# Kernel tuning notes

Hardware: AMD Instinct MI355X
Metric: run time of the kernel (lower is better)

Reference implementation:

```python
import jax, jax.numpy as jnp
import numpy as np

# opt constants baked from init_kwargs
OPT_M = 1024      # number of OFDM subcarriers (opt.M)
N_PILOT = 0       # opt.N_pilot
VELOCITY = 100.0  # opt.V (is_random_v=False)
DECAY = 4.0       # opt.decay
C_LIGHT = 3.0e8
CARRIER_FREQ = 3.0e9


def setup_inputs() -> dict:
    key = jax.random.key(0)
    k1, k2 = jax.random.split(key, 2)
    N, P, L, M, S = 16, 4, 16, OPT_M, 128
    # channel tap power profile: exp(-l/decay), normalized
    power = jnp.exp(-jnp.arange(L, dtype=jnp.float32) / DECAY)
    power = power / jnp.sum(power)
    # Rayleigh(sigma=1) samples = sqrt(g1^2 + g2^2), g_i ~ N(0,1)
    g = jax.random.normal(k1, (N, P, L, 2), dtype=jnp.float32)
    rayleigh = jnp.sqrt(g[..., 0] ** 2 + g[..., 1] ** 2)
    cof = jnp.sqrt(power / 2.0) * rayleigh  # (N,P,L), strictly positive
    input_ri = jax.random.normal(k2, (N, P, S * M, 2), dtype=jnp.float32)
    return {"input_ri": input_ri, "cof": cof, "Ns": 128}


def reference(input_ri, cof, Ns):
    N, P, SMK, _ = input_ri.shape
    L = cof.shape[-1]
    S = Ns + N_PILOT  # OFDM mode: S = Ns + N_pilot, M = opt.M
    Mk = SMK // S
    x = (input_ri[..., 0] + 1j * input_ri[..., 1]).astype(jnp.complex64)  # (N,P,SMK)

    # per-tap propagation delay from tap gain: len = -100*log(cof); delay1 = len/c
    delay1 = (-100.0 * jnp.log(cof)) / C_LIGHT                      # (N,P,L)
    delay2 = jnp.linspace(0.0, (S - 1) * (0.0005 / 14.0), S).astype(jnp.float32)  # (S,)
    delay = delay1[..., None] + delay2                              # (N,P,L,S)

    max_doppler = VELOCITY / C_LIGHT * CARRIER_FREQ
    angles = jnp.linspace(0.0, 2.0 * np.pi, L).astype(jnp.float32)  # (L,)
    phase_coef = (2.0 * np.pi * jnp.cos(angles) * max_doppler)      # (L,)
    phases = phase_coef[None, None, :, None] * delay                # (N,P,L,S)
    shift = jnp.exp(-1j * phases.astype(jnp.float32))               # complex64 (N,P,L,S)

    # sum over taps L BEFORE multiplying by the L-independent input (same math,
    # avoids materializing the (N,P,L,S,M) broadcast intermediate)
    factor = jnp.sum(cof[..., None].astype(jnp.complex64) * shift, axis=2)  # (N,P,S)
    out = x.reshape(N, P, S, Mk) * factor[..., None]                # (N,P,S,M)
    out = out.reshape(N, P, SMK)
    out_ri = jnp.stack([out.real, out.imag], axis=-1)               # (N,P,SMK,2)

    # frequency response H_t = FFT of zero-padded taps
    cof_zp = jnp.concatenate([cof, jnp.zeros((N, P, OPT_M - L), cof.dtype)], axis=-1)
    H_t = jnp.fft.fft(cof_zp.astype(jnp.complex64), axis=-1)        # (N,P,OPT_M)
    H_t_ri = jnp.stack([H_t.real, H_t.imag], axis=-1)
    return out_ri, H_t_ri
```

## Files before the change

### kernel.cpp

```cpp
#include <hip/hip_runtime.h>
#include <math.h>

#define NB     16
#define PB     4
#define LTAPS  16
#define SS     128
#define MM     1024

#define TWO_PI_F 6.28318530717958647692f

#define HT_BLKS     256
#define STREAM_BLKS 2048
#define TOT4 (NB * PB * SS * MM / 2)

typedef float f32x4 __attribute__((ext_vector_type(4)));
typedef float f32x2 __attribute__((ext_vector_type(2)));

__global__ __launch_bounds__(256) void fused_kernel(
    const float* __restrict__ in,
    const float* __restrict__ cof,
    float* __restrict__ out,
    float* __restrict__ ht)
{
    const int b = blockIdx.x;
    const int t = threadIdx.x;

    if (b >= HT_BLKS) {
        const int sb = b - HT_BLKS;
        __shared__ float term_re[64], term_im[64];
        __shared__ f32x2 facs[4];

        if (t < 64) {
            const int j  = t >> 4;
            const int l  = t & 15;
            const int id = sb * 4 + j;
            const int np = id >> 7;
            const int s  = id & (SS - 1);
            const float cofl   = cof[np * LTAPS + l];
            const float delay1 = (-100.0f / 3.0e8f) * logf(cofl);
            const float delay2 = (0.0005f / 14.0f) * (float)s;
            const float pc     = TWO_PI_F * 1000.0f * cosf((TWO_PI_F / 15.0f) * (float)l);
            const float ph     = pc * (delay1 + delay2);
            float sn, cs;
            sincosf(ph, &sn, &cs);
            term_re[t] = cofl * cs;
            term_im[t] = -cofl * sn;
        }
        __syncthreads();
        if (t < 4) {
            float re = 0.0f, im = 0.0f;
#pragma unroll
            for (int l = 0; l < LTAPS; ++l) {
                re += term_re[t * 16 + l];
                im += term_im[t * 16 + l];
            }
            f32x2 f; f.x = re; f.y = im;
            facs[t] = f;
        }
        __syncthreads();

        const f32x4* __restrict__ in4  = (const f32x4*)in + (size_t)sb * 2048;
        f32x4* __restrict__       out4 = (f32x4*)out      + (size_t)sb * 2048;
#pragma unroll
        for (int k = 0; k < 8; ++k) {
            const int   idx = k * 256 + t;
            const f32x2 f   = facs[k >> 1];
            const f32x4 v   = __builtin_nontemporal_load(&in4[idx]);
            f32x4 r;
            r.x = v.x * f.x - v.y * f.y;
            r.y = v.x * f.y + v.y * f.x;
            r.z = v.z * f.x - v.w * f.y;
            r.w = v.z * f.y + v.w * f.x;
            __builtin_nontemporal_store(r, &out4[idx]);
        }
    } else {
        const int id = b * 256 + t;
        const int np = id >> 10;
        const int k  = id & (MM - 1);
        float sn, cs;
        sincosf((TWO_PI_F / (float)MM) * (float)k, &sn, &cs);
        const float wr = cs, wi = -sn;
        const float* __restrict__ c = cof + np * LTAPS;
        float hr = 0.0f, hi = 0.0f;
        float cr = 1.0f, ci = 0.0f;
#pragma unroll
        for (int l = 0; l < LTAPS; ++l) {
            const float cl = c[l];
            hr += cl * cr;
            hi += cl * ci;
            const float nr = cr * wr - ci * wi;
            const float ni = cr * wi + ci * wr;
            cr = nr; ci = ni;
        }
        float2* __restrict__ o = (float2*)ht;
        o[id] = make_float2(hr, hi);
    }
}

extern "C" void kernel_launch(void* const* d_in, const int* in_sizes, int n_in,
                              void* d_out, int out_size, void* d_ws, size_t ws_size,
                              hipStream_t stream)
{
    const float* in  = (const float*)d_in[0];
    const float* cof = (const float*)d_in[1];
    float* out = (float*)d_out;
    float* ht  = out + (size_t)NB * PB * SS * MM * 2;

    hipLaunchKernelGGL(fused_kernel, dim3(HT_BLKS + STREAM_BLKS), dim3(256), 0, stream,
                       in, cof, out, ht);
}
```

Before: 26.59 us.

## Issue input loads before factor computation and replace LDS reduction with wave shuffles

Each streaming block now issues all eight nontemporal 16-byte loads up front, then has every wavefront redundantly compute the four per-symbol tap sums with xor-shuffle reductions instead of shared memory and two barriers. This overlaps the transcendental factor computation with memory latency and removes block-wide synchronisation. The cost is redundant log/sincos work in all four waves and more live registers to hold the loaded vectors.

```diff
diff --git a/kernel.cpp b/kernel.cpp
--- a/kernel.cpp
+++ b/kernel.cpp
@@ -14,7 +14,6 @@
 #define TOT4 (NB * PB * SS * MM / 2)
 
 typedef float f32x4 __attribute__((ext_vector_type(4)));
-typedef float f32x2 __attribute__((ext_vector_type(2)));
 
 __global__ __launch_bounds__(256) void fused_kernel(
     const float* __restrict__ in,
@@ -27,51 +26,50 @@
 
     if (b >= HT_BLKS) {
         const int sb = b - HT_BLKS;
-        __shared__ float term_re[64], term_im[64];
-        __shared__ f32x2 facs[4];
-
-        if (t < 64) {
-            const int j  = t >> 4;
-            const int l  = t & 15;
-            const int id = sb * 4 + j;
-            const int np = id >> 7;
-            const int s  = id & (SS - 1);
-            const float cofl   = cof[np * LTAPS + l];
-            const float delay1 = (-100.0f / 3.0e8f) * logf(cofl);
-            const float delay2 = (0.0005f / 14.0f) * (float)s;
-            const float pc     = TWO_PI_F * 1000.0f * cosf((TWO_PI_F / 15.0f) * (float)l);
-            const float ph     = pc * (delay1 + delay2);
-            float sn, cs;
-            sincosf(ph, &sn, &cs);
-            term_re[t] = cofl * cs;
-            term_im[t] = -cofl * sn;
-        }
-        __syncthreads();
-        if (t < 4) {
-            float re = 0.0f, im = 0.0f;
-#pragma unroll
-            for (int l = 0; l < LTAPS; ++l) {
-                re += term_re[t * 16 + l];
-                im += term_im[t * 16 + l];
-            }
-            f32x2 f; f.x = re; f.y = im;
-            facs[t] = f;
-        }
-        __syncthreads();
 
         const f32x4* __restrict__ in4  = (const f32x4*)in + (size_t)sb * 2048;
         f32x4* __restrict__       out4 = (f32x4*)out      + (size_t)sb * 2048;
+        f32x4 v[8];
+#pragma unroll
+        for (int k = 0; k < 8; ++k)
+            v[k] = __builtin_nontemporal_load(&in4[k * 256 + t]);
+
+        const int lane = t & 63;
+        const int j    = lane >> 4;
+        const int l    = lane & 15;
+        const int id   = sb * 4 + j;
+        const int np   = id >> 7;
+        const int s    = id & (SS - 1);
+        const float cofl   = cof[np * LTAPS + l];
+        const float delay1 = (-100.0f / 3.0e8f) * logf(cofl);
+        const float delay2 = (0.0005f / 14.0f) * (float)s;
+        const float pc     = TWO_PI_F * 1000.0f * cosf((TWO_PI_F / 15.0f) * (float)l);
+        const float ph     = pc * (delay1 + delay2);
+        float sn, cs;
+        sincosf(ph, &sn, &cs);
+        float re = cofl * cs;
+        float im = -cofl * sn;
+#pragma unroll
+        for (int w = 1; w < 16; w <<= 1) {
+            re += __shfl_xor(re, w);
+            im += __shfl_xor(im, w);
+        }
+        float fre[4], fim[4];
+#pragma unroll
+        for (int jj = 0; jj < 4; ++jj) {
+            fre[jj] = __shfl(re, jj * 16);
+            fim[jj] = __shfl(im, jj * 16);
+        }
+
 #pragma unroll
         for (int k = 0; k < 8; ++k) {
-            const int   idx = k * 256 + t;
-            const f32x2 f   = facs[k >> 1];
-            const f32x4 v   = __builtin_nontemporal_load(&in4[idx]);
+            const int jj = k >> 1;
             f32x4 r;
-            r.x = v.x * f.x - v.y * f.y;
-            r.y = v.x * f.y + v.y * f.x;
-            r.z = v.z * f.x - v.w * f.y;
-            r.w = v.z * f.y + v.w * f.x;
-            __builtin_nontemporal_store(r, &out4[idx]);
+            r.x = v[k].x * fre[jj] - v[k].y * fim[jj];
+            r.y = v[k].x * fim[jj] + v[k].y * fre[jj];
+            r.z = v[k].z * fre[jj] - v[k].w * fim[jj];
+            r.w = v[k].z * fim[jj] + v[k].w * fre[jj];
+            __builtin_nontemporal_store(r, &out4[k * 256 + t]);
         }
     } else {
         const int id = b * 256 + t;
```

New measurement: 25.63 us, median of 2. -3.6%, faster.
